# Optimization experiments

Measured on AMD Instinct MI355X. Metric: run time of the kernel, lower is better.

## Reference

```python
import jax, jax.numpy as jnp
import numpy as np

N, C, T, V = 16, 64, 512, 25
R, O, S = 8, 64, 3  # rel_channels, out_channels, num_subset


def setup_inputs() -> dict:
    key = jax.random.key(0)
    ks = jax.random.split(key, 12)
    sc = 0.05
    return {
        "x": jax.random.normal(ks[0], (N, C, T, V), jnp.float32),
        "A": jax.random.normal(ks[1], (S, V, V), jnp.float32) * 0.1,
        "alpha": jax.random.normal(ks[2], (1,), jnp.float32) * 0.1,
        "w1": jax.random.normal(ks[3], (S, R, C), jnp.float32) * sc,
        "b1": jax.random.normal(ks[4], (S, R), jnp.float32) * sc,
        "w2": jax.random.normal(ks[5], (S, R, C), jnp.float32) * sc,
        "b2": jax.random.normal(ks[6], (S, R), jnp.float32) * sc,
        "w3": jax.random.normal(ks[7], (S, O, C), jnp.float32) * sc,
        "b3": jax.random.normal(ks[8], (S, O), jnp.float32) * sc,
        "w4": jax.random.normal(ks[9], (S, O, R), jnp.float32) * sc,
        "b4": jax.random.normal(ks[10], (S, O), jnp.float32) * sc,
        "sparse": 0,
    }


def _mask(w, thr):
    # SparseConv2d: magnitude-threshold the 1x1 conv weights at runtime.
    return jnp.where(jnp.abs(w) > thr, w, jnp.zeros_like(w))


def reference(x, A, alpha, w1, b1, w2, b2, w3, b3, w4, b4, sparse):
    thr = jnp.float32(sparse)

    def conv1x1(w, b, inp):  # w [o,c], b [o], inp [n,c,t,v] -> [n,o,t,v]
        return jnp.einsum('oc,nctv->notv', _mask(w, thr), inp) + b[None, :, None, None]

    y = None
    for i in range(A.shape[0]):
        x1 = conv1x1(w1[i], b1[i], x).mean(-2)          # [n,r,v]
        x2 = conv1x1(w2[i], b2[i], x).mean(-2)          # [n,r,v]
        x3 = conv1x1(w3[i], b3[i], x)                   # [n,o,t,v]
        att = jnp.tanh(x1[..., :, None] - x2[..., None, :])  # [n,r,v,v]
        a = jnp.einsum('or,nruv->nouv', _mask(w4[i], thr), att) + b4[i][None, :, None, None]
        a = a * alpha + A[i][None, None]                # [n,o,v,v]
        z = jnp.einsum('ncuv,nctu->nctv', a, x3)        # node aggregation
        y = z if y is None else y + z
    # in_channels == out_channels -> residual is identity
    return jax.nn.relu(y + x)
```

## Files before the change

kernel.cpp:

```cpp
#include <hip/hip_runtime.h>
#include <cmath>

typedef __bf16 bf16x4v __attribute__((ext_vector_type(4)));
typedef __bf16 bf16x8 __attribute__((ext_vector_type(8)));
typedef float f32x4 __attribute__((ext_vector_type(4)));

namespace {
constexpr int kN = 16, kC = 64, kT = 512, kV = 25, kS = 3, kO = 64;
constexpr int kTV = kT * kV;
constexpr size_t WS_AFRAG = 102400;
constexpr size_t WS_W3F = WS_AFRAG + (size_t)48 * 131072;
}

__device__ __forceinline__ int swzB(int c, int t, int ubyte) {
  return (c << 9) + (((t << 6) + ubyte) ^ ((((c ^ t) & 7)) << 4));
}

__global__ __launch_bounds__(256) void k1_mean(const float* __restrict__ x,
                                               float* __restrict__ xm) {
  const int bid = blockIdx.x;
  __shared__ float part[250][4];
  const int tid = threadIdx.x;
  const float4* xg4 = (const float4*)(x + (size_t)bid * kTV);
  if (tid < 250) {
    float a0 = 0.f, a1 = 0.f, a2 = 0.f, a3 = 0.f;
    for (int j = tid; j < 3200; j += 250) {
      float4 v = xg4[j];
      a0 += v.x; a1 += v.y; a2 += v.z; a3 += v.w;
    }
    part[tid][0] = a0; part[tid][1] = a1; part[tid][2] = a2; part[tid][3] = a3;
  }
  __syncthreads();
  if (tid < 25) {
    float s = 0.f;
#pragma unroll
    for (int r = 0; r < 4; ++r) {
      int q = ((tid - r + 25) % 25) * 19 % 25;
#pragma unroll
      for (int p = 0; p < 10; ++p) s += part[q + 25 * p][r];
    }
    xm[bid * 25 + tid] = s * (1.f / 512.f);
  }
}

__global__ __launch_bounds__(256) void k2_attn(
    const float* __restrict__ xm, const float* __restrict__ Ag,
    const float* __restrict__ alpha, const float* __restrict__ w1,
    const float* __restrict__ b1, const float* __restrict__ w2,
    const float* __restrict__ b2, const float* __restrict__ w3,
    const float* __restrict__ w4, const float* __restrict__ b4,
    const int* __restrict__ sparse, unsigned char* __restrict__ ws) {
  const float thr = (float)sparse[0];
  const int b = blockIdx.x;
  const int s = b >> 6, n = (b >> 2) & 15, q = b & 3;
  __shared__ float xm_l[1600];
  __shared__ float x1_l[200], x2_l[200];
  __shared__ float att_l[8 * 625];
  __shared__ float attsum_l[200];
  __shared__ float ag_l[625];
  __shared__ float acs_l[25];
  __shared__ float w4_l[512];
  const int tid = threadIdx.x;
  for (int i = tid; i < 1600; i += 256) xm_l[i] = xm[n * 1600 + i];
  for (int i = tid; i < 512; i += 256) {
    float w = w4[s * 512 + i];
    w4_l[i] = (fabsf(w) > thr) ? w : 0.f;
  }
  for (int i = tid; i < 625; i += 256) ag_l[i] = Ag[s * 625 + i];
  __syncthreads();
  for (int i = tid; i < 400; i += 256) {
    int which = i / 200, idx = i % 200, r = idx / 25, u = idx % 25;
    const float* wrow = (which == 0 ? w1 : w2) + (s * 8 + r) * 64;
    float acc = 0.f;
    for (int cc = 0; cc < 64; ++cc) {
      float w = wrow[cc];
      w = (fabsf(w) > thr) ? w : 0.f;
      acc += w * xm_l[cc * 25 + u];
    }
    acc += (which == 0 ? b1 : b2)[s * 8 + r];
    if (which == 0) x1_l[idx] = acc;
    else x2_l[idx] = acc;
  }
  __syncthreads();
  for (int i = tid; i < 8 * 625; i += 256) {
    int r = i / 625, uv = i % 625, u = uv / 25, v = uv % 25;
    att_l[i] = tanhf(x1_l[r * 25 + u] - x2_l[r * 25 + v]);
  }
  __syncthreads();
  if (tid < 200) {
    int r = tid / 25, v = tid % 25;
    float sum = 0.f;
    for (int u = 0; u < 25; ++u) sum += att_l[r * 625 + u * 25 + v];
    attsum_l[tid] = sum;
  } else if (tid < 225) {
    int v = tid - 200;
    float sum = 0.f;
    for (int u = 0; u < 25; ++u) sum += ag_l[u * 25 + v];
    acs_l[v] = sum;
  }
  __syncthreads();
  const float al = alpha[0];
  unsigned char* afrag = ws + WS_AFRAG + (size_t)(s * 16 + n) * 131072;
  for (int slot = q * 2048 + tid; slot < (q + 1) * 2048; slot += 256) {
    int c = slot >> 7, vt = (slot >> 6) & 1, l = slot & 63;
    int v = vt * 16 + (l & 15), g = l >> 4;
    bf16x8 out;
    if (v < 25) {
      float b4v = b4[s * 64 + c];
#pragma unroll
      for (int j = 0; j < 8; ++j) {
        int u = g * 8 + j;
        float val = 0.f;
        if (u < 25) {
          float acc = 0.f;
#pragma unroll
          for (int r = 0; r < 8; ++r) acc += w4_l[c * 8 + r] * att_l[r * 625 + u * 25 + v];
          val = al * (acc + b4v) + ag_l[u * 25 + v];
        } else if (u == 25) {
          float acc = 0.f;
#pragma unroll
          for (int r = 0; r < 8; ++r) acc += w4_l[c * 8 + r] * attsum_l[r * 25 + v];
          val = al * acc + 25.f * al * b4v + acs_l[v];
        }
        out[j] = (__bf16)val;
      }
    } else {
#pragma unroll
      for (int j = 0; j < 8; ++j) out[j] = (__bf16)0.f;
    }
    *(bf16x8*)(afrag + (size_t)slot * 16) = out;
  }
  if (n == 0 && tid < 128) {
    unsigned char* w3f = ws + WS_W3F + (size_t)s * 8192;
    int slot = q * 128 + tid;
    int ot = slot >> 7, ks = (slot >> 6) & 1, l = slot & 63;
    int o = ot * 16 + (l & 15), g = l >> 4;
    bf16x8 out;
#pragma unroll
    for (int j = 0; j < 8; ++j) {
      int cp = ks * 32 + g * 8 + j;
      float w = w3[(s * 64 + o) * 64 + cp];
      out[j] = (__bf16)((fabsf(w) > thr) ? w : 0.f);
    }
    *(bf16x8*)(w3f + slot * 16) = out;
  }
}

__global__ __launch_bounds__(512) void k3_main(const float* __restrict__ x,
                                               const float* __restrict__ b3,
                                               const unsigned char* __restrict__ ws,
                                               float* __restrict__ y) {
  const int n = blockIdx.x;
  const int tb = blockIdx.y;
  extern __shared__ __align__(16) unsigned char smem[];
  const int tid = threadIdx.x;
  const int w = tid >> 6, l = tid & 63, g = l >> 4, l15 = l & 15;
  const float4* xg4 = (const float4*)(x + (size_t)n * kC * kTV);

  for (int idx = tid; idx < 1536; idx += 512) {
    int pair = idx / 3, k = idx % 3;
    int c = pair >> 3, t = pair & 7;
    *(unsigned int*)(smem + swzB(c, t, 52 + 4 * k)) = 0u;
  }

  bf16x8 xa[2][2];
#pragma unroll
  for (int cti = 0; cti < 2; ++cti)
#pragma unroll
    for (int kf = 0; kf < 2; ++kf)
#pragma unroll
      for (int j = 0; j < 8; ++j) xa[cti][kf][j] = (__bf16)0.f;
  {
    const float* xb = x + (size_t)n * kC * kTV + (tb * 8 + w) * 25;
#pragma unroll
    for (int cti = 0; cti < 2; ++cti) {
      int u = cti * 16 + l15;
      if (u < 25) {
#pragma unroll
        for (int kf = 0; kf < 2; ++kf)
#pragma unroll
          for (int j = 0; j < 8; ++j) {
            int cp = kf * 32 + g * 8 + j;
            xa[cti][kf][j] = (__bf16)xb[(size_t)cp * kTV + u];
          }
      }
    }
  }

  const unsigned char* afrag = ws + WS_AFRAG;
  const unsigned char* w3f = ws + WS_W3F;

  f32x4 zacc[8][2];
#pragma unroll
  for (int cc = 0; cc < 8; ++cc)
#pragma unroll
    for (int vt = 0; vt < 2; ++vt) {
      f32x4 zz = {0.f, 0.f, 0.f, 0.f};
      zacc[cc][vt] = zz;
    }

  for (int s = 0; s < kS; ++s) {
    if (s) __syncthreads();
#pragma unroll
    for (int ot = 0; ot < 4; ++ot) {
      bf16x8 wk0 = *(const bf16x8*)(w3f + s * 8192 + ((ot * 2 + 0) * 64 + l) * 16);
      bf16x8 wk1 = *(const bf16x8*)(w3f + s * 8192 + ((ot * 2 + 1) * 64 + l) * 16);
      f32x4 d0 = {0.f, 0.f, 0.f, 0.f}, d1 = {0.f, 0.f, 0.f, 0.f};
      d0 = __builtin_amdgcn_mfma_f32_16x16x32_bf16(xa[0][0], wk0, d0, 0, 0, 0);
      d0 = __builtin_amdgcn_mfma_f32_16x16x32_bf16(xa[0][1], wk1, d0, 0, 0, 0);
      d1 = __builtin_amdgcn_mfma_f32_16x16x32_bf16(xa[1][0], wk0, d1, 0, 0, 0);
      d1 = __builtin_amdgcn_mfma_f32_16x16x32_bf16(xa[1][1], wk1, d1, 0, 0, 0);
      int c = ot * 16 + l15;
      {
        bf16x4v pk;
        pk[0] = (__bf16)d0[0]; pk[1] = (__bf16)d0[1];
        pk[2] = (__bf16)d0[2]; pk[3] = (__bf16)d0[3];
        *(bf16x4v*)(smem + swzB(c, w, g * 8)) = pk;
      }
      if (g < 2) {
        bf16x4v pk;
        pk[0] = (__bf16)d1[0]; pk[1] = (__bf16)d1[1];
        pk[2] = (__bf16)d1[2]; pk[3] = (__bf16)d1[3];
        *(bf16x4v*)(smem + swzB(c, w, 32 + g * 8)) = pk;
      } else if (g == 2) {
        *(__bf16*)(smem + swzB(c, w, 48)) = (__bf16)d1[0];
      }
    }
    {
      int c = tid >> 3, t = tid & 7;
      *(__bf16*)(smem + swzB(c, t, 50)) = (__bf16)b3[s * 64 + c];
    }
    const unsigned char* af = afrag + (size_t)(s * 16 + n) * 131072;
    bf16x8 b2cur0 = *(const bf16x8*)(af + ((w * 8 * 2 + 0) * 64 + l) * 16);
    bf16x8 b2cur1 = *(const bf16x8*)(af + ((w * 8 * 2 + 1) * 64 + l) * 16);
    __syncthreads();
#pragma unroll
    for (int cc = 0; cc < 8; ++cc) {
      int c = w * 8 + cc;
      bf16x8 b2n0, b2n1;
      if (cc < 7) {
        b2n0 = *(const bf16x8*)(af + (((c + 1) * 2 + 0) * 64 + l) * 16);
        b2n1 = *(const bf16x8*)(af + (((c + 1) * 2 + 1) * 64 + l) * 16);
      }
      bf16x8 a2 = *(const bf16x8*)(smem + swzB(c, l15 & 7, g * 16));
      zacc[cc][0] = __builtin_amdgcn_mfma_f32_16x16x32_bf16(a2, b2cur0, zacc[cc][0], 0, 0, 0);
      zacc[cc][1] = __builtin_amdgcn_mfma_f32_16x16x32_bf16(a2, b2cur1, zacc[cc][1], 0, 0, 0);
      if (cc < 7) {
        b2cur0 = b2n0;
        b2cur1 = b2n1;
      }
    }
  }
  float* zs = (float*)(smem + 32768);
  float4* yg4 = (float4*)(y + (size_t)n * kC * kTV);
#pragma unroll
  for (int h = 0; h < 2; ++h) {
    if ((w >> 2) == h && g < 2) {
      int c0l = (w & 3) * 8;
#pragma unroll
      for (int cc = 0; cc < 8; ++cc)
#pragma unroll
        for (int vt = 0; vt < 2; ++vt) {
          int v = vt * 16 + l15;
          if (v < 25) {
#pragma unroll
            for (int jj = 0; jj < 4; ++jj)
              zs[(c0l + cc) * 200 + (g * 4 + jj) * 25 + v] = zacc[cc][vt][jj];
          }
        }
    }
    __syncthreads();
    for (int i4 = tid; i4 < 1600; i4 += 512) {
      int cl = i4 / 50, r4 = i4 % 50, c = h * 32 + cl;
      float4 xv = xg4[c * 3200 + tb * 50 + r4];
      f32x4 zv = *(const f32x4*)(zs + cl * 200 + r4 * 4);
      float4 o;
      o.x = fmaxf(zv[0] + xv.x, 0.f);
      o.y = fmaxf(zv[1] + xv.y, 0.f);
      o.z = fmaxf(zv[2] + xv.z, 0.f);
      o.w = fmaxf(zv[3] + xv.w, 0.f);
      yg4[c * 3200 + tb * 50 + r4] = o;
    }
    __syncthreads();
  }
}

extern "C" void kernel_launch(void* const* d_in, const int* in_sizes, int n_in,
                              void* d_out, int out_size, void* d_ws, size_t ws_size,
                              hipStream_t stream) {
  const float* x = (const float*)d_in[0];
  const float* Ag = (const float*)d_in[1];
  const float* alpha = (const float*)d_in[2];
  const float* w1 = (const float*)d_in[3];
  const float* b1 = (const float*)d_in[4];
  const float* w2 = (const float*)d_in[5];
  const float* b2 = (const float*)d_in[6];
  const float* w3 = (const float*)d_in[7];
  const float* b3 = (const float*)d_in[8];
  const float* w4 = (const float*)d_in[9];
  const float* b4 = (const float*)d_in[10];
  const int* sparse = (const int*)d_in[11];

  unsigned char* ws = (unsigned char*)d_ws;
  float* xm = (float*)ws;
  float* y = (float*)d_out;

  hipFuncSetAttribute((const void*)k3_main,
                      hipFuncAttributeMaxDynamicSharedMemorySize, 65536);

  k1_mean<<<kN * kC, 256, 0, stream>>>(x, xm);
  k2_attn<<<kS * kN * 4, 256, 0, stream>>>(xm, Ag, alpha, w1, b1, w2, b2, w3, w4,
                                           b4, sparse, ws);
  dim3 g3(kN, kT / 8);
  k3_main<<<g3, 512, 58368, stream>>>(x, b3, ws, y);
}
```

Baseline: 92.28 us.

## Pre-transpose x to bf16 channel-last and restructure main kernel per-warp channels

```diff
diff --git a/kernel.cpp b/kernel.cpp
--- a/kernel.cpp
+++ b/kernel.cpp
@@ -10,36 +10,64 @@
 constexpr int kTV = kT * kV;
 constexpr size_t WS_AFRAG = 102400;
 constexpr size_t WS_W3F = WS_AFRAG + (size_t)48 * 131072;
-}
-
-__device__ __forceinline__ int swzB(int c, int t, int ubyte) {
-  return (c << 9) + (((t << 6) + ubyte) ^ ((((c ^ t) & 7)) << 4));
-}
-
-__global__ __launch_bounds__(256) void k1_mean(const float* __restrict__ x,
-                                               float* __restrict__ xm) {
-  const int bid = blockIdx.x;
-  __shared__ float part[250][4];
+constexpr size_t WS_XTR = WS_W3F + 3 * 8192;
+constexpr size_t WS_PSUM = WS_XTR + (size_t)16 * 819200 * 2 + 4096;
+}
+
+__device__ __forceinline__ int swzC(int c, int t, int ubyte) {
+  return (c << 10) + (((t << 6) + ubyte) ^ ((((c ^ t) & 7)) << 4));
+}
+
+__global__ __launch_bounds__(512) void k1_tr(const float* __restrict__ x,
+                                             unsigned char* __restrict__ ws) {
+  const int n = blockIdx.x, tc = blockIdx.y;
+  extern __shared__ __align__(16) unsigned char sm1[];
+  __bf16* tile = (__bf16*)sm1;
   const int tid = threadIdx.x;
-  const float4* xg4 = (const float4*)(x + (size_t)bid * kTV);
-  if (tid < 250) {
-    float a0 = 0.f, a1 = 0.f, a2 = 0.f, a3 = 0.f;
-    for (int j = tid; j < 3200; j += 250) {
-      float4 v = xg4[j];
-      a0 += v.x; a1 += v.y; a2 += v.z; a3 += v.w;
-    }
-    part[tid][0] = a0; part[tid][1] = a1; part[tid][2] = a2; part[tid][3] = a3;
-  }
-  __syncthreads();
-  if (tid < 25) {
+  const float4* xg4 = (const float4*)(x + (size_t)n * kC * kTV);
+  for (int i4 = tid; i4 < 12800; i4 += 512) {
+    int c = i4 / 200, r = i4 % 200;
+    float4 v = xg4[c * 3200 + tc * 200 + r];
+    bf16x4v o;
+    o[0] = (__bf16)v.x; o[1] = (__bf16)v.y;
+    o[2] = (__bf16)v.z; o[3] = (__bf16)v.w;
+    *(bf16x4v*)(tile + c * 800 + r * 4) = o;
+  }
+  __syncthreads();
+  __bf16* xtr = (__bf16*)(ws + WS_XTR) + (size_t)n * 819200 + (size_t)tc * 51200;
+  for (int col = tid; col < 800; col += 512) {
+    __bf16* dst = xtr + (size_t)col * 64;
+#pragma unroll
+    for (int cb = 0; cb < 8; ++cb) {
+      bf16x8 pk;
+#pragma unroll
+      for (int j = 0; j < 8; ++j) pk[j] = tile[(cb * 8 + j) * 800 + col];
+      *(bf16x8*)(dst + cb * 8) = pk;
+    }
+  }
+  float* psum = (float*)(ws + WS_PSUM);
+  for (int i = tid; i < 1600; i += 512) {
+    int c = i / 25, v = i % 25;
     float s = 0.f;
 #pragma unroll
-    for (int r = 0; r < 4; ++r) {
-      int q = ((tid - r + 25) % 25) * 19 % 25;
-#pragma unroll
-      for (int p = 0; p < 10; ++p) s += part[q + 25 * p][r];
-    }
-    xm[bid * 25 + tid] = s * (1.f / 512.f);
+    for (int t = 0; t < 32; ++t) s += (float)tile[c * 800 + t * 25 + v];
+    psum[((size_t)n * 1600 + i) * 16 + tc] = s;
+  }
+}
+
+__global__ __launch_bounds__(256) void k1_red(const unsigned char* __restrict__ ws_c,
+                                              float* __restrict__ xm) {
+  const float* psum = (const float*)(ws_c + WS_PSUM);
+  const int n = blockIdx.x, tid = threadIdx.x;
+  for (int i = tid; i < 1600; i += 256) {
+    const float4* p = (const float4*)(psum + ((size_t)n * 1600 + i) * 16);
+    float s = 0.f;
+#pragma unroll
+    for (int q = 0; q < 4; ++q) {
+      float4 v = p[q];
+      s += v.x + v.y + v.z + v.w;
+    }
+    xm[n * 1600 + i] = s * (1.f / 512.f);
   }
 }
 
@@ -146,7 +174,8 @@
   }
 }
 
-__global__ __launch_bounds__(512) void k3_main(const float* __restrict__ x,
+__global__ __launch_bounds__(256) void k3_main(const float* __restrict__ x,
+                                               const __bf16* __restrict__ xtr,
                                                const float* __restrict__ b3,
                                                const unsigned char* __restrict__ ws,
                                                float* __restrict__ y) {
@@ -155,133 +184,126 @@
   extern __shared__ __align__(16) unsigned char smem[];
   const int tid = threadIdx.x;
   const int w = tid >> 6, l = tid & 63, g = l >> 4, l15 = l & 15;
-  const float4* xg4 = (const float4*)(x + (size_t)n * kC * kTV);
-
-  for (int idx = tid; idx < 1536; idx += 512) {
+  const int co = w * 16;
+
+  for (int idx = l; idx < 768; idx += 64) {
     int pair = idx / 3, k = idx % 3;
-    int c = pair >> 3, t = pair & 7;
-    *(unsigned int*)(smem + swzB(c, t, 52 + 4 * k)) = 0u;
-  }
-
-  bf16x8 xa[2][2];
-#pragma unroll
-  for (int cti = 0; cti < 2; ++cti)
-#pragma unroll
-    for (int kf = 0; kf < 2; ++kf)
-#pragma unroll
-      for (int j = 0; j < 8; ++j) xa[cti][kf][j] = (__bf16)0.f;
-  {
-    const float* xb = x + (size_t)n * kC * kTV + (tb * 8 + w) * 25;
-#pragma unroll
-    for (int cti = 0; cti < 2; ++cti) {
-      int u = cti * 16 + l15;
-      if (u < 25) {
-#pragma unroll
-        for (int kf = 0; kf < 2; ++kf)
-#pragma unroll
-          for (int j = 0; j < 8; ++j) {
-            int cp = kf * 32 + g * 8 + j;
-            xa[cti][kf][j] = (__bf16)xb[(size_t)cp * kTV + u];
-          }
-      }
-    }
-  }
-
+    int cl = pair >> 4, t = pair & 15;
+    *(unsigned int*)(smem + swzC(co + cl, t, 52 + 4 * k)) = 0u;
+  }
+
+  const unsigned char* w3f = ws + WS_W3F;
+  bf16x8 wk00 = *(const bf16x8*)(w3f + 0 * 8192 + ((w * 2 + 0) * 64 + l) * 16);
+  bf16x8 wk01 = *(const bf16x8*)(w3f + 0 * 8192 + ((w * 2 + 1) * 64 + l) * 16);
+  bf16x8 wk10 = *(const bf16x8*)(w3f + 1 * 8192 + ((w * 2 + 0) * 64 + l) * 16);
+  bf16x8 wk11 = *(const bf16x8*)(w3f + 1 * 8192 + ((w * 2 + 1) * 64 + l) * 16);
+  bf16x8 wk20 = *(const bf16x8*)(w3f + 2 * 8192 + ((w * 2 + 0) * 64 + l) * 16);
+  bf16x8 wk21 = *(const bf16x8*)(w3f + 2 * 8192 + ((w * 2 + 1) * 64 + l) * 16);
+  float b3v0 = b3[0 * 64 + co + (l & 15)];
+  float b3v1 = b3[1 * 64 + co + (l & 15)];
+  float b3v2 = b3[2 * 64 + co + (l & 15)];
+
+  const __bf16* xt = xtr + (size_t)n * 819200 + (size_t)tb * 400 * 64;
   const unsigned char* afrag = ws + WS_AFRAG;
-  const unsigned char* w3f = ws + WS_W3F;
-
-  f32x4 zacc[8][2];
-#pragma unroll
-  for (int cc = 0; cc < 8; ++cc)
+
+  f32x4 zacc[16][2];
+#pragma unroll
+  for (int cc = 0; cc < 16; ++cc)
 #pragma unroll
     for (int vt = 0; vt < 2; ++vt) {
       f32x4 zz = {0.f, 0.f, 0.f, 0.f};
       zacc[cc][vt] = zz;
     }
 
+#pragma unroll
   for (int s = 0; s < kS; ++s) {
-    if (s) __syncthreads();
-#pragma unroll
-    for (int ot = 0; ot < 4; ++ot) {
-      bf16x8 wk0 = *(const bf16x8*)(w3f + s * 8192 + ((ot * 2 + 0) * 64 + l) * 16);
-      bf16x8 wk1 = *(const bf16x8*)(w3f + s * 8192 + ((ot * 2 + 1) * 64 + l) * 16);
+    const bf16x8 wks0 = (s == 0) ? wk00 : (s == 1) ? wk10 : wk20;
+    const bf16x8 wks1 = (s == 0) ? wk01 : (s == 1) ? wk11 : wk21;
+    const float b3vs = (s == 0) ? b3v0 : (s == 1) ? b3v1 : b3v2;
+#pragma unroll
+    for (int t = 0; t < 16; ++t) {
+      const __bf16* bp = xt + (size_t)t * 1600;
+      bf16x8 xa00 = *(const bf16x8*)(bp + l15 * 64 + g * 8);
+      bf16x8 xa01 = *(const bf16x8*)(bp + l15 * 64 + 32 + g * 8);
+      bf16x8 xa10 = *(const bf16x8*)(bp + (16 + l15) * 64 + g * 8);
+      bf16x8 xa11 = *(const bf16x8*)(bp + (16 + l15) * 64 + 32 + g * 8);
       f32x4 d0 = {0.f, 0.f, 0.f, 0.f}, d1 = {0.f, 0.f, 0.f, 0.f};
-      d0 = __builtin_amdgcn_mfma_f32_16x16x32_bf16(xa[0][0], wk0, d0, 0, 0, 0);
-      d0 = __builtin_amdgcn_mfma_f32_16x16x32_bf16(xa[0][1], wk1, d0, 0, 0, 0);
-      d1 = __builtin_amdgcn_mfma_f32_16x16x32_bf16(xa[1][0], wk0, d1, 0, 0, 0);
-      d1 = __builtin_amdgcn_mfma_f32_16x16x32_bf16(xa[1][1], wk1, d1, 0, 0, 0);
-      int c = ot * 16 + l15;
+      d0 = __builtin_amdgcn_mfma_f32_16x16x32_bf16(xa00, wks0, d0, 0, 0, 0);
+      d0 = __builtin_amdgcn_mfma_f32_16x16x32_bf16(xa01, wks1, d0, 0, 0, 0);
+      d1 = __builtin_amdgcn_mfma_f32_16x16x32_bf16(xa10, wks0, d1, 0, 0, 0);
+      d1 = __builtin_amdgcn_mfma_f32_16x16x32_bf16(xa11, wks1, d1, 0, 0, 0);
+      int c = co + l15;
       {
         bf16x4v pk;
         pk[0] = (__bf16)d0[0]; pk[1] = (__bf16)d0[1];
         pk[2] = (__bf16)d0[2]; pk[3] = (__bf16)d0[3];
-        *(bf16x4v*)(smem + swzB(c, w, g * 8)) = pk;
+        *(bf16x4v*)(smem + swzC(c, t, g * 8)) = pk;
       }
       if (g < 2) {
         bf16x4v pk;
         pk[0] = (__bf16)d1[0]; pk[1] = (__bf16)d1[1];
         pk[2] = (__bf16)d1[2]; pk[3] = (__bf16)d1[3];
-        *(bf16x4v*)(smem + swzB(c, w, 32 + g * 8)) = pk;
+        *(bf16x4v*)(smem + swzC(c, t, 32 + g * 8)) = pk;
       } else if (g == 2) {
-        *(__bf16*)(smem + swzB(c, w, 48)) = (__bf16)d1[0];
-      }
-    }
-    {
-      int c = tid >> 3, t = tid & 7;
-      *(__bf16*)(smem + swzB(c, t, 50)) = (__bf16)b3[s * 64 + c];
-    }
+        *(__bf16*)(smem + swzC(c, t, 48)) = (__bf16)d1[0];
+      }
+    }
+#pragma unroll
+    for (int k = 0; k < 4; ++k)
+      *(__bf16*)(smem + swzC(co + (l & 15), (l >> 4) + 4 * k, 50)) = (__bf16)b3vs;
     const unsigned char* af = afrag + (size_t)(s * 16 + n) * 131072;
-    bf16x8 b2cur0 = *(const bf16x8*)(af + ((w * 8 * 2 + 0) * 64 + l) * 16);
-    bf16x8 b2cur1 = *(const bf16x8*)(af + ((w * 8 * 2 + 1) * 64 + l) * 16);
-    __syncthreads();
+    bf16x8 cur0 = *(const bf16x8*)(af + ((co * 2 + 0) * 64 + l) * 16);
+    bf16x8 cur1 = *(const bf16x8*)(af + ((co * 2 + 1) * 64 + l) * 16);
+    bf16x8 nxt0 = *(const bf16x8*)(af + (((co + 1) * 2 + 0) * 64 + l) * 16);
+    bf16x8 nxt1 = *(const bf16x8*)(af + (((co + 1) * 2 + 1) * 64 + l) * 16);
+#pragma unroll
+    for (int cc = 0; cc < 16; ++cc) {
+      bf16x8 f0, f1;
+      if (cc < 14) {
+        f0 = *(const bf16x8*)(af + (((co + cc + 2) * 2 + 0) * 64 + l) * 16);
+        f1 = *(const bf16x8*)(af + (((co + cc + 2) * 2 + 1) * 64 + l) * 16);
+      }
+      bf16x8 a2 = *(const bf16x8*)(smem + swzC(co + cc, l15, g * 16));
+      zacc[cc][0] = __builtin_amdgcn_mfma_f32_16x16x32_bf16(a2, cur0, zacc[cc][0], 0, 0, 0);
+      zacc[cc][1] = __builtin_amdgcn_mfma_f32_16x16x32_bf16(a2, cur1, zacc[cc][1], 0, 0, 0);
+      if (cc < 14) {
+        cur0 = nxt0; cur1 = nxt1;
+        nxt0 = f0; nxt1 = f1;
+      } else {
+        cur0 = nxt0; cur1 = nxt1;
+      }
+    }
+  }
+
+  float* zs = (float*)(smem + w * 16384);
+  const float4* xg4 = (const float4*)(x + (size_t)n * kC * kTV);
+  float4* yg4 = (float4*)(y + (size_t)n * kC * kTV);
+#pragma unroll
+  for (int hh = 0; hh < 2; ++hh) {
 #pragma unroll
     for (int cc = 0; cc < 8; ++cc) {
-      int c = w * 8 + cc;
-      bf16x8 b2n0, b2n1;
-      if (cc < 7) {
-        b2n0 = *(const bf16x8*)(af + (((c + 1) * 2 + 0) * 64 + l) * 16);
-        b2n1 = *(const bf16x8*)(af + (((c + 1) * 2 + 1) * 64 + l) * 16);
-      }
-      bf16x8 a2 = *(const bf16x8*)(smem + swzB(c, l15 & 7, g * 16));
-      zacc[cc][0] = __builtin_amdgcn_mfma_f32_16x16x32_bf16(a2, b2cur0, zacc[cc][0], 0, 0, 0);
-      zacc[cc][1] = __builtin_amdgcn_mfma_f32_16x16x32_bf16(a2, b2cur1, zacc[cc][1], 0, 0, 0);
-      if (cc < 7) {
-        b2cur0 = b2n0;
-        b2cur1 = b2n1;
-      }
-    }
-  }
-  float* zs = (float*)(smem + 32768);
-  float4* yg4 = (float4*)(y + (size_t)n * kC * kTV);
-#pragma unroll
-  for (int h = 0; h < 2; ++h) {
-    if ((w >> 2) == h && g < 2) {
-      int c0l = (w & 3) * 8;
-#pragma unroll
-      for (int cc = 0; cc < 8; ++cc)
-#pragma unroll
-        for (int vt = 0; vt < 2; ++vt) {
-          int v = vt * 16 + l15;
-          if (v < 25) {
-#pragma unroll
-            for (int jj = 0; jj < 4; ++jj)
-              zs[(c0l + cc) * 200 + (g * 4 + jj) * 25 + v] = zacc[cc][vt][jj];
-          }
+#pragma unroll
+      for (int vt = 0; vt < 2; ++vt) {
+        int v = vt * 16 + l15;
+        if (v < 25) {
+#pragma unroll
+          for (int jj = 0; jj < 4; ++jj)
+            zs[cc * 400 + (g * 4 + jj) * 25 + v] = zacc[hh * 8 + cc][vt][jj];
         }
-    }
-    __syncthreads();
-    for (int i4 = tid; i4 < 1600; i4 += 512) {
-      int cl = i4 / 50, r4 = i4 % 50, c = h * 32 + cl;
-      float4 xv = xg4[c * 3200 + tb * 50 + r4];
-      f32x4 zv = *(const f32x4*)(zs + cl * 200 + r4 * 4);
+      }
+    }
+    for (int i4 = l; i4 < 800; i4 += 64) {
+      int ccl = i4 / 100, r4 = i4 % 100;
+      int cg = co + hh * 8 + ccl;
+      f32x4 zv = *(const f32x4*)(zs + ccl * 400 + r4 * 4);
+      float4 xv = xg4[cg * 3200 + tb * 100 + r4];
       float4 o;
       o.x = fmaxf(zv[0] + xv.x, 0.f);
       o.y = fmaxf(zv[1] + xv.y, 0.f);
       o.z = fmaxf(zv[2] + xv.z, 0.f);
       o.w = fmaxf(zv[3] + xv.w, 0.f);
-      yg4[c * 3200 + tb * 50 + r4] = o;
-    }
-    __syncthreads();
+      yg4[cg * 3200 + tb * 100 + r4] = o;
+    }
   }
 }
 
@@ -303,14 +325,19 @@
 
   unsigned char* ws = (unsigned char*)d_ws;
   float* xm = (float*)ws;
+  const __bf16* xtr = (const __bf16*)(ws + WS_XTR);
   float* y = (float*)d_out;
 
+  hipFuncSetAttribute((const void*)k1_tr,
+                      hipFuncAttributeMaxDynamicSharedMemorySize, 102400);
   hipFuncSetAttribute((const void*)k3_main,
                       hipFuncAttributeMaxDynamicSharedMemorySize, 65536);
 
-  k1_mean<<<kN * kC, 256, 0, stream>>>(x, xm);
+  dim3 g1(kN, kT / 32);
+  k1_tr<<<g1, 512, 102400, stream>>>(x, ws);
+  k1_red<<<kN, 256, 0, stream>>>(ws, xm);
   k2_attn<<<kS * kN * 4, 256, 0, stream>>>(xm, Ag, alpha, w1, b1, w2, b2, w3, w4,
                                            b4, sparse, ws);
-  dim3 g3(kN, kT / 8);
-  k3_main<<<g3, 512, 58368, stream>>>(x, b3, ws, y);
-}
+  dim3 g3(kN, kT / 16);
+  k3_main<<<g3, 256, 65536, stream>>>(x, (const __bf16*)xtr, b3, ws, y);
+}
```

Measured after the change: 135.5 us. 1.47x slower.
